# Performance work log

Measured on AMD Instinct MI355X. Metric: run time of the kernel, lower is better.

## Reference

```python
import jax, jax.numpy as jnp
import numpy as np
from jax import lax

B, T, C = 8, 2048, 1024
H, N = 16, 64          # n_head, head_size (C = H*N)
FFN = 3584             # dim_ffn = int(1024*3.5//32*32)
HSD = 8.0              # head_size_divisor
EPS = 1e-5


def setup_inputs() -> dict:
    key = jax.random.key(0)
    ks = jax.random.split(key, 24)
    s = 0.02
    return {
        'x': jax.random.normal(ks[0], (B, T, C), jnp.float32),
        'ln0_w': jnp.ones((C,), jnp.float32), 'ln0_b': jnp.zeros((C,), jnp.float32),
        'ln1_w': jnp.ones((C,), jnp.float32), 'ln1_b': jnp.zeros((C,), jnp.float32),
        'ln2_w': jnp.ones((C,), jnp.float32), 'ln2_b': jnp.zeros((C,), jnp.float32),
        'att_tmk': jax.random.uniform(ks[1], (C,), jnp.float32),
        'att_tmv': jax.random.uniform(ks[2], (C,), jnp.float32),
        'att_tmr': jax.random.uniform(ks[3], (C,), jnp.float32),
        'att_tmg': jax.random.uniform(ks[4], (C,), jnp.float32),
        'att_decay': jax.random.uniform(ks[5], (H, N), jnp.float32, -6.0, -1.0),
        'att_faaaa': jax.random.normal(ks[6], (H, N), jnp.float32) * 0.1,
        'att_Wr': jax.random.normal(ks[7], (C, C), jnp.float32) * s,
        'att_Wk': jax.random.normal(ks[8], (C, C), jnp.float32) * s,
        'att_Wv': jax.random.normal(ks[9], (C, C), jnp.float32) * s,
        'att_Wg': jax.random.normal(ks[10], (C, C), jnp.float32) * s,
        'att_Wo': jax.random.normal(ks[11], (C, C), jnp.float32) * s,
        'att_lnx_w': jnp.ones((C,), jnp.float32), 'att_lnx_b': jnp.zeros((C,), jnp.float32),
        'ffn_tmk': jax.random.uniform(ks[12], (C,), jnp.float32),
        'ffn_tmr': jax.random.uniform(ks[13], (C,), jnp.float32),
        'ffn_Wk': jax.random.normal(ks[14], (FFN, C), jnp.float32) * s,
        'ffn_Wr': jax.random.normal(ks[15], (C, C), jnp.float32) * s,
        'ffn_Wv': jax.random.normal(ks[16], (C, FFN), jnp.float32) * s,
    }


def token_shift(x):
    # nn.ZeroPad2d((0,0,1,-1)): shift right by one along T with zero front pad
    return jnp.pad(x, ((0, 0), (1, 0), (0, 0)))[:, :-1, :]


def layer_norm(x, w, b):
    mu = jnp.mean(x, -1, keepdims=True)
    var = jnp.var(x, -1, keepdims=True)
    return (x - mu) * lax.rsqrt(var + EPS) * w + b


def group_norm(x, w, b):
    # GroupNorm(H groups) over channel dim C = H*N
    xg = x.reshape(*x.shape[:-1], H, N)
    mu = jnp.mean(xg, -1, keepdims=True)
    var = jnp.var(xg, -1, keepdims=True)
    xg = (xg - mu) * lax.rsqrt(var + EPS)
    return xg.reshape(x.shape) * w + b


def wkv5(r, k, v, w, u):
    # r,k,v: [B,T,C]; w,u: [H,N]. Per-head decayed linear attention recurrence.
    ew = jnp.exp(-jnp.exp(w))  # [H,N] decay in (0,1)
    rt = r.reshape(B, T, H, N).transpose(1, 0, 2, 3)  # [T,B,H,N]
    kt = k.reshape(B, T, H, N).transpose(1, 0, 2, 3)
    vt = v.reshape(B, T, H, N).transpose(1, 0, 2, 3)

    def step(S, rkv):
        r_, k_, v_ = rkv                                   # [B,H,N]
        a = k_[..., :, None] * v_[..., None, :]            # [B,H,N,N] outer k v^T
        y = jnp.einsum('bhi,bhij->bhj', r_, S + u[:, :, None] * a)
        S = ew[None, :, :, None] * S + a
        return S, y

    S0 = jnp.zeros((B, H, N, N), r.dtype)
    _, ys = lax.scan(step, S0, (rt, kt, vt))               # ys: [T,B,H,N]
    return ys.transpose(1, 0, 2, 3).reshape(B, T, C)


def reference(x, ln0_w, ln0_b, ln1_w, ln1_b, ln2_w, ln2_b,
              att_tmk, att_tmv, att_tmr, att_tmg, att_decay, att_faaaa,
              att_Wr, att_Wk, att_Wv, att_Wg, att_Wo, att_lnx_w, att_lnx_b,
              ffn_tmk, ffn_tmr, ffn_Wk, ffn_Wr, ffn_Wv):
    x = layer_norm(x, ln0_w, ln0_b)  # layer_id == 0

    # --- time-mix (RWKV_Tmix_x052) ---
    xn = layer_norm(x, ln1_w, ln1_b)
    xx = token_shift(xn)
    xk = xn * att_tmk + xx * (1 - att_tmk)
    xv = xn * att_tmv + xx * (1 - att_tmv)
    xr = xn * att_tmr + xx * (1 - att_tmr)
    xg = xn * att_tmg + xx * (1 - att_tmg)
    r = xr @ att_Wr.T
    k = xk @ att_Wk.T
    v = xv @ att_Wv.T
    g = jax.nn.silu(xg @ att_Wg.T)
    y = wkv5(r, k, v, att_decay, att_faaaa)
    y = group_norm(y / HSD, att_lnx_w, att_lnx_b)
    x = x + (y * g) @ att_Wo.T

    # --- channel-mix (RWKV_CMix_x052) ---
    xn = layer_norm(x, ln2_w, ln2_b)
    xx = token_shift(xn)
    xk = xn * ffn_tmk + xx * (1 - ffn_tmk)
    xr = xn * ffn_tmr + xx * (1 - ffn_tmr)
    kf = jnp.square(jax.nn.relu(xk @ ffn_Wk.T))
    kv = kf @ ffn_Wv.T
    x = x + jax.nn.sigmoid(xr @ ffn_Wr.T) * kv
    return x
```

## Files before the change

### kernel.cpp

```cpp
#include <hip/hip_runtime.h>

#define Bq 8
#define Tq 2048
#define Cq 1024
#define Hq 16
#define Nq 64
#define FFNq 3584
#define EPSq 1e-5f

typedef __bf16 bf8v __attribute__((ext_vector_type(8)));
typedef float f32x4 __attribute__((ext_vector_type(4)));

typedef __attribute__((address_space(1))) const unsigned int GU;
typedef __attribute__((address_space(3))) unsigned int LU;

__device__ __forceinline__ void gload16(const unsigned short* g, unsigned short* l) {
    __builtin_amdgcn_global_load_lds((GU*)g, (LU*)l, 16, 0, 0);
}

__device__ __forceinline__ unsigned short f2bf(float f) {
    unsigned u = __float_as_uint(f);
    u += 0x7fffu + ((u >> 16) & 1u);
    return (unsigned short)(u >> 16);
}
__device__ __forceinline__ float bf2f(unsigned short h) {
    return __uint_as_float(((unsigned)h) << 16);
}

__global__ __launch_bounds__(256)
void diag_kernel(float* __restrict__ out, float val) {
    int i = (blockIdx.x * 256 + threadIdx.x) * 4;
    float4 v = make_float4(val, val, val, val);
    *(float4*)(out + i) = v;
}

__global__ __launch_bounds__(256)
void f2bf_all_kernel(const float* __restrict__ s0, const float* __restrict__ s1,
                     const float* __restrict__ s2, const float* __restrict__ s3,
                     const float* __restrict__ s4, const float* __restrict__ s5,
                     const float* __restrict__ s6, const float* __restrict__ s7,
                     unsigned short* __restrict__ d0, unsigned short* __restrict__ d1,
                     unsigned short* __restrict__ d2, unsigned short* __restrict__ d3,
                     unsigned short* __restrict__ d4, unsigned short* __restrict__ d5,
                     unsigned short* __restrict__ d6, unsigned short* __restrict__ d7) {
    int b = blockIdx.x;
    const float* src; unsigned short* dst;
    if      (b < 1024)  { src = s0; dst = d0; }
    else if (b < 2048)  { src = s1; dst = d1; b -= 1024; }
    else if (b < 3072)  { src = s2; dst = d2; b -= 2048; }
    else if (b < 4096)  { src = s3; dst = d3; b -= 3072; }
    else if (b < 5120)  { src = s4; dst = d4; b -= 4096; }
    else if (b < 8704)  { src = s5; dst = d5; b -= 5120; }
    else if (b < 9728)  { src = s6; dst = d6; b -= 8704; }
    else                { src = s7; dst = d7; b -= 9728; }
    int i = (b * 256 + threadIdx.x) * 4;
    float4 v = *(const float4*)(src + i);
    ushort4 o;
    o.x = f2bf(v.x); o.y = f2bf(v.y); o.z = f2bf(v.z); o.w = f2bf(v.w);
    *(ushort4*)(dst + i) = o;
}

__device__ __forceinline__ void blockred2(float& a, float& b, float* sm) {
#pragma unroll
    for (int m = 1; m < 64; m <<= 1) { a += __shfl_xor(a, m); b += __shfl_xor(b, m); }
    const int w = threadIdx.x >> 6;
    __syncthreads();
    if ((threadIdx.x & 63) == 0) { sm[w] = a; sm[4 + w] = b; }
    __syncthreads();
    a = sm[0] + sm[1] + sm[2] + sm[3];
    b = sm[4] + sm[5] + sm[6] + sm[7];
}

__global__ __launch_bounds__(256)
void ln01_kernel(const float* __restrict__ x,
                 const float* __restrict__ w0, const float* __restrict__ b0,
                 const float* __restrict__ w1, const float* __restrict__ b1,
                 float* __restrict__ x0, unsigned short* __restrict__ xn) {
    __shared__ float sm[8];
    const int tok = blockIdx.x, tid = threadIdx.x, c = tid * 4;
    const size_t base = (size_t)tok * Cq + c;
    float4 v = *(const float4*)(x + base);
    float s = v.x + v.y + v.z + v.w;
    float ss = v.x * v.x + v.y * v.y + v.z * v.z + v.w * v.w;
    blockred2(s, ss, sm);
    float mu = s * (1.f / Cq);
    float rstd = rsqrtf(ss * (1.f / Cq) - mu * mu + EPSq);
    float4 wv = *(const float4*)(w0 + c), bv = *(const float4*)(b0 + c);
    float4 e;
    e.x = (v.x - mu) * rstd * wv.x + bv.x;
    e.y = (v.y - mu) * rstd * wv.y + bv.y;
    e.z = (v.z - mu) * rstd * wv.z + bv.z;
    e.w = (v.w - mu) * rstd * wv.w + bv.w;
    *(float4*)(x0 + base) = e;
    s = e.x + e.y + e.z + e.w;
    ss = e.x * e.x + e.y * e.y + e.z * e.z + e.w * e.w;
    blockred2(s, ss, sm);
    mu = s * (1.f / Cq);
    rstd = rsqrtf(ss * (1.f / Cq) - mu * mu + EPSq);
    wv = *(const float4*)(w1 + c); bv = *(const float4*)(b1 + c);
    ushort4 o;
    o.x = f2bf((e.x - mu) * rstd * wv.x + bv.x);
    o.y = f2bf((e.y - mu) * rstd * wv.y + bv.y);
    o.z = f2bf((e.z - mu) * rstd * wv.z + bv.z);
    o.w = f2bf((e.w - mu) * rstd * wv.w + bv.w);
    *(ushort4*)(xn + base) = o;
}

__global__ __launch_bounds__(256)
void ln_kernel(const float* __restrict__ x, const float* __restrict__ w,
               const float* __restrict__ b, unsigned short* __restrict__ out) {
    __shared__ float sm[8];
    const int tok = blockIdx.x, tid = threadIdx.x, c = tid * 4;
    const size_t base = (size_t)tok * Cq + c;
    float4 v = *(const float4*)(x + base);
    float s = v.x + v.y + v.z + v.w;
    float ss = v.x * v.x + v.y * v.y + v.z * v.z + v.w * v.w;
    blockred2(s, ss, sm);
    float mu = s * (1.f / Cq);
    float rstd = rsqrtf(ss * (1.f / Cq) - mu * mu + EPSq);
    float4 wv = *(const float4*)(w + c), bv = *(const float4*)(b + c);
    ushort4 o;
    o.x = f2bf((v.x - mu) * rstd * wv.x + bv.x);
    o.y = f2bf((v.y - mu) * rstd * wv.y + bv.y);
    o.z = f2bf((v.z - mu) * rstd * wv.z + bv.z);
    o.w = f2bf((v.w - mu) * rstd * wv.w + bv.w);
    *(ushort4*)(out + base) = o;
}

__device__ __forceinline__ ushort4 mixpack(float ax, float ay, float az, float aw,
                                           float px, float py, float pz, float pw,
                                           const float4& m) {
    ushort4 o;
    o.x = f2bf(px + m.x * (ax - px));
    o.y = f2bf(py + m.y * (ay - py));
    o.z = f2bf(pz + m.z * (az - pz));
    o.w = f2bf(pw + m.w * (aw - pw));
    return o;
}

__global__ __launch_bounds__(256)
void mix4_kernel(const unsigned short* __restrict__ xn,
                 const float* __restrict__ tmr, const float* __restrict__ tmk,
                 const float* __restrict__ tmv, const float* __restrict__ tmg,
                 ushort4* __restrict__ outR, ushort4* __restrict__ outK,
                 ushort4* __restrict__ outV, ushort4* __restrict__ outG) {
    const int tok = blockIdx.x, tid = threadIdx.x, c = tid * 4;
    const int t = tok & (Tq - 1);
    const size_t base = (size_t)tok * Cq + c;
    ushort4 a = *(const ushort4*)(xn + base);
    ushort4 p = make_ushort4(0, 0, 0, 0);
    if (t) p = *(const ushort4*)(xn + base - Cq);
    float ax = bf2f(a.x), ay = bf2f(a.y), az = bf2f(a.z), aw = bf2f(a.w);
    float px = bf2f(p.x), py = bf2f(p.y), pz = bf2f(p.z), pw = bf2f(p.w);
    const size_t b4 = (size_t)tok * 256 + tid;
    outR[b4] = mixpack(ax, ay, az, aw, px, py, pz, pw, *(const float4*)(tmr + c));
    outK[b4] = mixpack(ax, ay, az, aw, px, py, pz, pw, *(const float4*)(tmk + c));
    outV[b4] = mixpack(ax, ay, az, aw, px, py, pz, pw, *(const float4*)(tmv + c));
    outG[b4] = mixpack(ax, ay, az, aw, px, py, pz, pw, *(const float4*)(tmg + c));
}

__global__ __launch_bounds__(256)
void mix2_kernel(const unsigned short* __restrict__ xn,
                 const float* __restrict__ tmk, const float* __restrict__ tmr,
                 ushort4* __restrict__ outK, ushort4* __restrict__ outR) {
    const int tok = blockIdx.x, tid = threadIdx.x, c = tid * 4;
    const int t = tok & (Tq - 1);
    const size_t base = (size_t)tok * Cq + c;
    ushort4 a = *(const ushort4*)(xn + base);
    ushort4 p = make_ushort4(0, 0, 0, 0);
    if (t) p = *(const ushort4*)(xn + base - Cq);
    float ax = bf2f(a.x), ay = bf2f(a.y), az = bf2f(a.z), aw = bf2f(a.w);
    float px = bf2f(p.x), py = bf2f(p.y), pz = bf2f(p.z), pw = bf2f(p.w);
    const size_t b4 = (size_t)tok * 256 + tid;
    outK[b4] = mixpack(ax, ay, az, aw, px, py, pz, pw, *(const float4*)(tmk + c));
    outR[b4] = mixpack(ax, ay, az, aw, px, py, pz, pw, *(const float4*)(tmr + c));
}

template<int MODE>
__global__ __launch_bounds__(256, 2)
void gemm_bt(const unsigned short* __restrict__ A, const unsigned short* __restrict__ W,
             int K, int N, float* __restrict__ outF, unsigned short* __restrict__ outB,
             const float* __restrict__ res, const unsigned short* __restrict__ sg) {
    __shared__ unsigned short As[128 * 32];
    __shared__ unsigned short Bs[128 * 32];
    const int tid = threadIdx.x;
    const int nn = N >> 7;
    const int per = nn << 4;
    const int gid = blockIdx.x / per;
    const int rem = blockIdx.x - gid * per;
    const int m0 = ((gid << 4) + (rem & 15)) * 128;
    const int n0 = (rem >> 4) * 128;
    const int wv = tid >> 6, lane = tid & 63;
    const int wm = (wv >> 1) * 64, wn = (wv & 1) * 64;
    const int l15 = lane & 15, q = lane >> 4;

    const int srow = wv * 32 + (lane >> 2);
    const int scol = (lane & 3) * 8;
    const unsigned short* Ag0 = A + (size_t)(m0 + srow) * K + scol;
    const unsigned short* Ag1 = A + (size_t)(m0 + srow + 16) * K + scol;
    const unsigned short* Wg0 = W + (size_t)(n0 + srow) * K + scol;
    const unsigned short* Wg1 = W + (size_t)(n0 + srow + 16) * K + scol;
    unsigned short* As0 = &As[(wv * 32) * 32];
    unsigned short* As1 = &As[(wv * 32 + 16) * 32];
    unsigned short* Bs0 = &Bs[(wv * 32) * 32];
    unsigned short* Bs1 = &Bs[(wv * 32 + 16) * 32];

    f32x4 acc[4][4];
#pragma unroll
    for (int mi = 0; mi < 4; ++mi)
#pragma unroll
        for (int ni = 0; ni < 4; ++ni)
            acc[mi][ni] = {0.f, 0.f, 0.f, 0.f};

    for (int k0 = 0; k0 < K; k0 += 32) {
        gload16(Ag0 + k0, As0);
        gload16(Ag1 + k0, As1);
        gload16(Wg0 + k0, Bs0);
        gload16(Wg1 + k0, Bs1);
        __syncthreads();
        bf8v af[4], bfv[4];
#pragma unroll
        for (int mi = 0; mi < 4; ++mi) af[mi] = *(const bf8v*)&As[(wm + mi * 16 + l15) * 32 + q * 8];
#pragma unroll
        for (int ni = 0; ni < 4; ++ni) bfv[ni] = *(const bf8v*)&Bs[(wn + ni * 16 + l15) * 32 + q * 8];
#pragma unroll
        for (int mi = 0; mi < 4; ++mi)
#pragma unroll
            for (int ni = 0; ni < 4; ++ni)
                acc[mi][ni] = __builtin_amdgcn_mfma_f32_16x16x32_bf16(af[mi], bfv[ni], acc[mi][ni], 0, 0, 0);
        __syncthreads();
    }

#pragma unroll
    for (int mi = 0; mi < 4; ++mi)
#pragma unroll
        for (int ni = 0; ni < 4; ++ni)
#pragma unroll
            for (int j = 0; j < 4; ++j) {
                const int row = m0 + wm + mi * 16 + q * 4 + j;
                const int col = n0 + wn + ni * 16 + l15;
                const size_t idx = (size_t)row * N + col;
                const float a = acc[mi][ni][j];
                if (MODE == 1) {
                    outB[idx] = f2bf(a / (1.f + __expf(-a)));
                } else if (MODE == 2) {
                    outF[idx] = res[idx] + a;
                } else if (MODE == 3) {
                    float t = fmaxf(a, 0.f);
                    outB[idx] = f2bf(t * t);
                } else if (MODE == 4) {
                    outB[idx] = f2bf(1.f / (1.f + __expf(-a)));
                } else if (MODE == 5) {
                    outF[idx] = res[idx] + bf2f(sg[idx]) * a;
                } else {
                    outB[idx] = f2bf(a);
                }
            }
}

__global__ __launch_bounds__(256)
void wkv_kernel(const unsigned short* __restrict__ r, const unsigned short* __restrict__ k,
                const unsigned short* __restrict__ v, const unsigned short* __restrict__ g,
                const float* __restrict__ decay, const float* __restrict__ faaaa,
                const float* __restrict__ lnxw, const float* __restrict__ lnxb,
                unsigned short* __restrict__ ao) {
    __shared__ unsigned short rp[64 * 72], km[64 * 72], kdT[64 * 72];
    __shared__ unsigned short VT[64 * 72], Abf[64 * 72], ScT[64 * 72], Gsh[64 * 72];
    __shared__ float Dt[64];
    const int tid = threadIdx.x;
    const int bh = blockIdx.x, b = bh >> 4, h = bh & 15;
    const int tr = tid >> 2, g4 = tid & 3, i0 = g4 * 16;
    const int wv = tid >> 6, lane = tid & 63, l15 = lane & 15, q = lane >> 4;
    const float LOG2E = 1.44269504088896340736f;

    float l2w[16], uu[16];
#pragma unroll
    for (int ii = 0; ii < 16; ++ii) {
        l2w[ii] = -__expf(decay[h * Nq + i0 + ii]) * LOG2E;
        uu[ii] = faaaa[h * Nq + i0 + ii];
    }
    float ewL[4];
#pragma unroll
    for (int jr = 0; jr < 4; ++jr) {
        float lw = -__expf(decay[h * Nq + 16 * wv + q * 4 + jr]) * LOG2E;
        ewL[jr] = exp2f(64.f * lw);
    }
    const int colbase = h * Nq;
    float lwj[4], lbj[4];
#pragma unroll
    for (int nt = 0; nt < 4; ++nt) {
        lwj[nt] = lnxw[colbase + 16 * nt + l15];
        lbj[nt] = lnxb[colbase + 16 * nt + l15];
    }
    f32x4 S[4];
#pragma unroll
    for (int nt = 0; nt < 4; ++nt) S[nt] = {0.f, 0.f, 0.f, 0.f};
    for (int idx = tid; idx < 64 * 72; idx += 256) ScT[idx] = 0;
    __syncthreads();

    const size_t rowbase = (size_t)b * Tq;

    for (int c = 0; c < 32; ++c) {
        const size_t grow = (rowbase + c * 64 + tr) * Cq + colbase + i0;
        unsigned short rs_[16], ks_[16], vs_[16];
        *(uint4*)&rs_[0] = *(const uint4*)(r + grow);
        *(uint4*)&rs_[8] = *(const uint4*)(r + grow + 8);
        *(uint4*)&ks_[0] = *(const uint4*)(k + grow);
        *(uint4*)&ks_[8] = *(const uint4*)(k + grow + 8);
        *(uint4*)&vs_[0] = *(const uint4*)(v + grow);
        *(uint4*)&vs_[8] = *(const uint4*)(v + grow + 8);
        *(uint4*)&Gsh[tr * 72 + i0] = *(const uint4*)(g + grow);
        *(uint4*)&Gsh[tr * 72 + i0 + 8] = *(const uint4*)(g + grow + 8);
        float pd = 0.f;
        const float ftr = (float)tr;
#pragma unroll
        for (int ii = 0; ii < 16; ++ii) {
            float rf = bf2f(rs_[ii]), kf = bf2f(ks_[ii]);
            rp[tr * 72 + i0 + ii] = f2bf(rf * exp2f(ftr * l2w[ii]));
            km[tr * 72 + i0 + ii] = f2bf(kf * exp2f(-(ftr + 1.f) * l2w[ii]));
            kdT[(i0 + ii) * 72 + tr] = f2bf(kf * exp2f((63.f - ftr) * l2w[ii]));
            VT[(i0 + ii) * 72 + tr] = vs_[ii];
            pd += rf * uu[ii] * kf;
        }
        pd += __shfl_xor(pd, 1);
        pd += __shfl_xor(pd, 2);
        if (g4 == 0) Dt[tr] = pd;
        __syncthreads();

        f32x4 accA[4];
#pragma unroll
        for (int nt = 0; nt < 4; ++nt) accA[nt] = {0.f, 0.f, 0.f, 0.f};
#pragma unroll
        for (int ks = 0; ks < 2; ++ks) {
            bf8v a = *(const bf8v*)&rp[(16 * wv + l15) * 72 + ks * 32 + q * 8];
#pragma unroll
            for (int nt = 0; nt < 4; ++nt) {
                bf8v bb = *(const bf8v*)&km[(16 * nt + l15) * 72 + ks * 32 + q * 8];
                accA[nt] = __builtin_amdgcn_mfma_f32_16x16x32_bf16(a, bb, accA[nt], 0, 0, 0);
            }
        }
#pragma unroll
        for (int nt = 0; nt < 4; ++nt)
#pragma unroll
            for (int jr = 0; jr < 4; ++jr) {
                const int t = 16 * wv + q * 4 + jr, s = 16 * nt + l15;
                const float a = accA[nt][jr];
                const float val = (s < t) ? a : ((s == t) ? Dt[t] : 0.f);
                Abf[t * 72 + s] = f2bf(val);
            }

        f32x4 accY[4];
#pragma unroll
        for (int nt = 0; nt < 4; ++nt) accY[nt] = {0.f, 0.f, 0.f, 0.f};
#pragma unroll
        for (int ks = 0; ks < 2; ++ks) {
            bf8v a = *(const bf8v*)&Abf[(16 * wv + l15) * 72 + ks * 32 + q * 8];
#pragma unroll
            for (int nt = 0; nt < 4; ++nt) {
                bf8v bb = *(const bf8v*)&VT[(16 * nt + l15) * 72 + ks * 32 + q * 8];
                accY[nt] = __builtin_amdgcn_mfma_f32_16x16x32_bf16(a, bb, accY[nt], 0, 0, 0);
            }
        }
#pragma unroll
        for (int ks = 0; ks < 2; ++ks) {
            bf8v a = *(const bf8v*)&rp[(16 * wv + l15) * 72 + ks * 32 + q * 8];
#pragma unroll
            for (int nt = 0; nt < 4; ++nt) {
                bf8v bb = *(const bf8v*)&ScT[(16 * nt + l15) * 72 + ks * 32 + q * 8];
                accY[nt] = __builtin_amdgcn_mfma_f32_16x16x32_bf16(a, bb, accY[nt], 0, 0, 0);
            }
        }

        float sum_[4] = {0.f, 0.f, 0.f, 0.f}, sq_[4] = {0.f, 0.f, 0.f, 0.f};
#pragma unroll
        for (int nt = 0; nt < 4; ++nt)
#pragma unroll
            for (int jr = 0; jr < 4; ++jr) {
                float yv = accY[nt][jr] * 0.125f;
                accY[nt][jr] = yv;
                sum_[jr] += yv;
                sq_[jr] += yv * yv;
            }
#pragma unroll
        for (int m = 1; m < 16; m <<= 1)
#pragma unroll
            for (int jr = 0; jr < 4; ++jr) {
                sum_[jr] += __shfl_xor(sum_[jr], m);
                sq_[jr] += __shfl_xor(sq_[jr], m);
            }
        float mu_[4], rstd_[4];
#pragma unroll
        for (int jr = 0; jr < 4; ++jr) {
            mu_[jr] = sum_[jr] * (1.f / Nq);
            rstd_[jr] = rsqrtf(sq_[jr] * (1.f / Nq) - mu_[jr] * mu_[jr] + EPSq);
        }
#pragma unroll
        for (int nt = 0; nt < 4; ++nt)
#pragma unroll
            for (int jr = 0; jr < 4; ++jr) {
                const int t = 16 * wv + q * 4 + jr;
                const float gate = bf2f(Gsh[t * 72 + 16 * nt + l15]);
                const float val = (accY[nt][jr] - mu_[jr]) * rstd_[jr] * lwj[nt] + lbj[nt];
                ao[(rowbase + c * 64 + t) * Cq + colbase + 16 * nt + l15] = f2bf(val * gate);
            }

        f32x4 accU[4];
#pragma unroll
        for (int nt = 0; nt < 4; ++nt) accU[nt] = {0.f, 0.f, 0.f, 0.f};
#pragma unroll
        for (int ks = 0; ks < 2; ++ks) {
            bf8v a = *(const bf8v*)&kdT[(16 * wv + l15) * 72 + ks * 32 + q * 8];
#pragma unroll
            for (int nt = 0; nt < 4; ++nt) {
                bf8v bb = *(const bf8v*)&VT[(16 * nt + l15) * 72 + ks * 32 + q * 8];
                accU[nt] = __builtin_amdgcn_mfma_f32_16x16x32_bf16(a, bb, accU[nt], 0, 0, 0);
            }
        }
        __syncthreads();
#pragma unroll
        for (int nt = 0; nt < 4; ++nt) {
#pragma unroll
            for (int jr = 0; jr < 4; ++jr)
                S[nt][jr] = ewL[jr] * S[nt][jr] + accU[nt][jr];
            ushort4 sc;
            sc.x = f2bf(S[nt][0]); sc.y = f2bf(S[nt][1]);
            sc.z = f2bf(S[nt][2]); sc.w = f2bf(S[nt][3]);
            *(ushort4*)&ScT[(16 * nt + l15) * 72 + 16 * wv + q * 4] = sc;
        }
        __syncthreads();
    }
}

extern "C" void kernel_launch(void* const* d_in, const int* in_sizes, int n_in,
                              void* d_out, int out_size, void* d_ws, size_t ws_size,
                              hipStream_t stream) {
    const float* x     = (const float*)d_in[0];
    const float* ln0w  = (const float*)d_in[1];
    const float* ln0b  = (const float*)d_in[2];
    const float* ln1w  = (const float*)d_in[3];
    const float* ln1b  = (const float*)d_in[4];
    const float* ln2w  = (const float*)d_in[5];
    const float* ln2b  = (const float*)d_in[6];
    const float* atmk  = (const float*)d_in[7];
    const float* atmv  = (const float*)d_in[8];
    const float* atmr  = (const float*)d_in[9];
    const float* atmg  = (const float*)d_in[10];
    const float* decay = (const float*)d_in[11];
    const float* faaaa = (const float*)d_in[12];
    const float* aWr   = (const float*)d_in[13];
    const float* aWk   = (const float*)d_in[14];
    const float* aWv   = (const float*)d_in[15];
    const float* aWg   = (const float*)d_in[16];
    const float* aWo   = (const float*)d_in[17];
    const float* lnxw  = (const float*)d_in[18];
    const float* lnxb  = (const float*)d_in[19];
    const float* ftmk  = (const float*)d_in[20];
    const float* ftmr  = (const float*)d_in[21];
    const float* fWk   = (const float*)d_in[22];
    const float* fWr   = (const float*)d_in[23];
    const float* fWv   = (const float*)d_in[24];

    const size_t MB = 1024ull * 1024ull;
    const size_t WS_NEEDED = 250 * MB;
    dim3 blk(256);

    if (ws_size < WS_NEEDED) {
        diag_kernel<<<out_size / 1024, blk, 0, stream>>>((float*)d_out,
            1000.f + (float)((double)ws_size / (double)MB));
        return;
    }

    char* ws = (char*)d_ws;
    unsigned short* WR  = (unsigned short*)(ws + 0 * MB);
    unsigned short* WK  = (unsigned short*)(ws + 2 * MB);
    unsigned short* WV  = (unsigned short*)(ws + 4 * MB);
    unsigned short* WG  = (unsigned short*)(ws + 6 * MB);
    unsigned short* WO  = (unsigned short*)(ws + 8 * MB);
    unsigned short* FWK = (unsigned short*)(ws + 10 * MB);
    unsigned short* FWR = (unsigned short*)(ws + 17 * MB);
    unsigned short* FWV = (unsigned short*)(ws + 19 * MB);
    unsigned short* XN  = (unsigned short*)(ws + 26 * MB);
    unsigned short* MXR = (unsigned short*)(ws + 58 * MB);
    unsigned short* MXK = (unsigned short*)(ws + 90 * MB);
    unsigned short* MXV = (unsigned short*)(ws + 122 * MB);
    unsigned short* MXG = (unsigned short*)(ws + 154 * MB);
    unsigned short* Rb  = (unsigned short*)(ws + 186 * MB);
    unsigned short* Kb  = (unsigned short*)(ws + 58 * MB);
    unsigned short* Vb  = (unsigned short*)(ws + 90 * MB);
    unsigned short* Gb  = (unsigned short*)(ws + 122 * MB);
    unsigned short* AO  = (unsigned short*)(ws + 154 * MB);
    unsigned short* XK2 = (unsigned short*)(ws + 58 * MB);
    unsigned short* XR2 = (unsigned short*)(ws + 90 * MB);
    unsigned short* KF  = (unsigned short*)(ws + 122 * MB);
    unsigned short* SRb = (unsigned short*)(ws + 26 * MB);
    float*          X0  = (float*)d_out;

    const int NTOK = Bq * Tq;
    dim3 g8(8 * 128), g28(28 * 128);

    f2bf_all_kernel<<<13312, blk, 0, stream>>>(aWr, aWk, aWv, aWg, aWo, fWk, fWr, fWv,
                                               WR, WK, WV, WG, WO, FWK, FWR, FWV);

    ln01_kernel<<<NTOK, blk, 0, stream>>>(x, ln0w, ln0b, ln1w, ln1b, X0, XN);

    mix4_kernel<<<NTOK, blk, 0, stream>>>(XN, atmr, atmk, atmv, atmg,
                                          (ushort4*)MXR, (ushort4*)MXK,
                                          (ushort4*)MXV, (ushort4*)MXG);
    gemm_bt<6><<<g8, blk, 0, stream>>>(MXR, WR, Cq, Cq, nullptr, Rb, nullptr, nullptr);
    gemm_bt<6><<<g8, blk, 0, stream>>>(MXK, WK, Cq, Cq, nullptr, Kb, nullptr, nullptr);
    gemm_bt<6><<<g8, blk, 0, stream>>>(MXV, WV, Cq, Cq, nullptr, Vb, nullptr, nullptr);
    gemm_bt<1><<<g8, blk, 0, stream>>>(MXG, WG, Cq, Cq, nullptr, Gb, nullptr, nullptr);

    wkv_kernel<<<Bq * Hq, blk, 0, stream>>>(Rb, Kb, Vb, Gb, decay, faaaa, lnxw, lnxb, AO);
    gemm_bt<2><<<g8, blk, 0, stream>>>(AO, WO, Cq, Cq, X0, nullptr, X0, nullptr);

    ln_kernel<<<NTOK, blk, 0, stream>>>(X0, ln2w, ln2b, XN);
    mix2_kernel<<<NTOK, blk, 0, stream>>>(XN, ftmk, ftmr, (ushort4*)XK2, (ushort4*)XR2);
    gemm_bt<3><<<g28, blk, 0, stream>>>(XK2, FWK, Cq, FFNq, nullptr, KF, nullptr, nullptr);
    gemm_bt<4><<<g8, blk, 0, stream>>>(XR2, FWR, Cq, Cq, nullptr, SRb, nullptr, nullptr);
    gemm_bt<5><<<g8, blk, 0, stream>>>(KF, FWV, FFNq, Cq, X0, nullptr, X0, SRb);
}
```

Measured before the change: 981.1 us.

## Replace GEMM with 256x256-tile, 4-stage pipelined, swizzled-LDS kernel

Swaps the 128x128 single-buffered GEMM for a 512-thread kernel using 256x256 output tiles, a 4-slot LDS ring that prefetches 3 K-steps ahead with explicit vmcnt waits, and an XOR swizzle on LDS columns to avoid bank conflicts. It also interleaves A/B loads with MFMA halves, raises wave priority around the MFMAs, and remaps block IDs for L2 locality. The aim is to hide global-load latency and cut LDS traffic per FLOP. In exchange it uses far more registers and LDS per block, giving lower occupancy and fewer blocks (256 for the square GEMMs) relative to the CU count.

```diff
diff --git a/kernel.cpp b/kernel.cpp
--- a/kernel.cpp
+++ b/kernel.cpp
@@ -177,68 +177,114 @@
 }
 
 template<int MODE>
-__global__ __launch_bounds__(256, 2)
-void gemm_bt(const unsigned short* __restrict__ A, const unsigned short* __restrict__ W,
+__global__ __launch_bounds__(512, 2)
+void gemm256(const unsigned short* __restrict__ A, const unsigned short* __restrict__ W,
              int K, int N, float* __restrict__ outF, unsigned short* __restrict__ outB,
              const float* __restrict__ res, const unsigned short* __restrict__ sg) {
-    __shared__ unsigned short As[128 * 32];
-    __shared__ unsigned short Bs[128 * 32];
+    __shared__ unsigned short lds[4][2][8192];
     const int tid = threadIdx.x;
-    const int nn = N >> 7;
-    const int per = nn << 4;
-    const int gid = blockIdx.x / per;
-    const int rem = blockIdx.x - gid * per;
-    const int m0 = ((gid << 4) + (rem & 15)) * 128;
-    const int n0 = (rem >> 4) * 128;
-    const int wv = tid >> 6, lane = tid & 63;
-    const int wm = (wv >> 1) * 64, wn = (wv & 1) * 64;
+    const int wid = tid >> 6, lane = tid & 63;
+    const int wr = wid >> 2, wc = wid & 3;
     const int l15 = lane & 15, q = lane >> 4;
 
-    const int srow = wv * 32 + (lane >> 2);
-    const int scol = (lane & 3) * 8;
-    const unsigned short* Ag0 = A + (size_t)(m0 + srow) * K + scol;
-    const unsigned short* Ag1 = A + (size_t)(m0 + srow + 16) * K + scol;
-    const unsigned short* Wg0 = W + (size_t)(n0 + srow) * K + scol;
-    const unsigned short* Wg1 = W + (size_t)(n0 + srow + 16) * K + scol;
-    unsigned short* As0 = &As[(wv * 32) * 32];
-    unsigned short* As1 = &As[(wv * 32 + 16) * 32];
-    unsigned short* Bs0 = &Bs[(wv * 32) * 32];
-    unsigned short* Bs1 = &Bs[(wv * 32 + 16) * 32];
-
-    f32x4 acc[4][4];
-#pragma unroll
-    for (int mi = 0; mi < 4; ++mi)
+    const int nn = N >> 8;
+    const int q8 = gridDim.x >> 3;
+    const int bid = blockIdx.x;
+    const int swz = (bid & 7) * q8 + (bid >> 3);
+    const int m0 = (swz / nn) * 256;
+    const int n0 = (swz % nn) * 256;
+
+    const int d0 = tid * 16, d1 = 8192 + tid * 16;
+    const int p0 = d0 ^ (((d0 >> 6) & 3) << 4);
+    const int p1 = d1 ^ (((d1 >> 6) & 3) << 4);
+    const int r0 = p0 >> 6, c0 = (p0 >> 1) & 31;
+    const int r1 = p1 >> 6, c1 = (p1 >> 1) & 31;
+    const unsigned short* a0 = A + (size_t)(m0 + r0) * K + c0;
+    const unsigned short* a1 = A + (size_t)(m0 + r1) * K + c1;
+    const unsigned short* w0 = W + (size_t)(n0 + r0) * K + c0;
+    const unsigned short* w1 = W + (size_t)(n0 + r1) * K + c1;
+
+    const int cOff = (q ^ (l15 & 3)) * 8;
+    const int aBase = (wr * 128 + l15) * 32 + cOff;
+    const int bBase = (wc * 64 + l15) * 32 + cOff;
+
+    f32x4 acc[8][4];
+#pragma unroll
+    for (int mi = 0; mi < 8; ++mi)
 #pragma unroll
         for (int ni = 0; ni < 4; ++ni)
             acc[mi][ni] = {0.f, 0.f, 0.f, 0.f};
 
-    for (int k0 = 0; k0 < K; k0 += 32) {
-        gload16(Ag0 + k0, As0);
-        gload16(Ag1 + k0, As1);
-        gload16(Wg0 + k0, Bs0);
-        gload16(Wg1 + k0, Bs1);
-        __syncthreads();
-        bf8v af[4], bfv[4];
-#pragma unroll
-        for (int mi = 0; mi < 4; ++mi) af[mi] = *(const bf8v*)&As[(wm + mi * 16 + l15) * 32 + q * 8];
-#pragma unroll
-        for (int ni = 0; ni < 4; ++ni) bfv[ni] = *(const bf8v*)&Bs[(wn + ni * 16 + l15) * 32 + q * 8];
+    const int NT = K >> 5;
+
+#pragma unroll
+    for (int t = 0; t < 3; ++t) {
+        unsigned short* La = (unsigned short*)&lds[t][0][wid * 512];
+        unsigned short* Lb = (unsigned short*)&lds[t][1][wid * 512];
+        gload16(a0, La); gload16(a1, La + 4096);
+        gload16(w0, Lb); gload16(w1, Lb + 4096);
+        a0 += 32; a1 += 32; w0 += 32; w1 += 32;
+    }
+    asm volatile("s_waitcnt vmcnt(8)" ::: "memory");
+    __builtin_amdgcn_s_barrier();
+
+    for (int t = 0; t < NT; ++t) {
+        const int slot = t & 3;
+        const bool st = (t + 3) < NT;
+        const int ps = (t + 3) & 3;
+        bf8v af[4], bb[4];
+
 #pragma unroll
         for (int mi = 0; mi < 4; ++mi)
+            af[mi] = *(const bf8v*)&lds[slot][0][aBase + mi * 512];
+#pragma unroll
+        for (int ni = 0; ni < 4; ++ni)
+            bb[ni] = *(const bf8v*)&lds[slot][1][bBase + ni * 512];
+        if (st) {
+            unsigned short* La = (unsigned short*)&lds[ps][0][wid * 512];
+            gload16(a0, La); gload16(a1, La + 4096);
+            a0 += 32; a1 += 32;
+        }
+        __builtin_amdgcn_s_barrier();
+        __builtin_amdgcn_s_setprio(1);
+#pragma unroll
+        for (int mi = 0; mi < 4; ++mi)
 #pragma unroll
             for (int ni = 0; ni < 4; ++ni)
-                acc[mi][ni] = __builtin_amdgcn_mfma_f32_16x16x32_bf16(af[mi], bfv[ni], acc[mi][ni], 0, 0, 0);
-        __syncthreads();
-    }
-
-#pragma unroll
-    for (int mi = 0; mi < 4; ++mi)
+                acc[mi][ni] = __builtin_amdgcn_mfma_f32_16x16x32_bf16(af[mi], bb[ni], acc[mi][ni], 0, 0, 0);
+        __builtin_amdgcn_s_setprio(0);
+        __builtin_amdgcn_s_barrier();
+
+#pragma unroll
+        for (int mi = 0; mi < 4; ++mi)
+            af[mi] = *(const bf8v*)&lds[slot][0][aBase + (4 + mi) * 512];
+        if (st) {
+            unsigned short* Lb = (unsigned short*)&lds[ps][1][wid * 512];
+            gload16(w0, Lb); gload16(w1, Lb + 4096);
+            w0 += 32; w1 += 32;
+        }
+        __builtin_amdgcn_s_barrier();
+        __builtin_amdgcn_s_setprio(1);
+#pragma unroll
+        for (int mi = 0; mi < 4; ++mi)
+#pragma unroll
+            for (int ni = 0; ni < 4; ++ni)
+                acc[4 + mi][ni] = __builtin_amdgcn_mfma_f32_16x16x32_bf16(af[mi], bb[ni], acc[4 + mi][ni], 0, 0, 0);
+        __builtin_amdgcn_s_setprio(0);
+        if (t < NT - 3)       { asm volatile("s_waitcnt vmcnt(8)" ::: "memory"); }
+        else if (t == NT - 3) { asm volatile("s_waitcnt vmcnt(4)" ::: "memory"); }
+        else if (t == NT - 2) { asm volatile("s_waitcnt vmcnt(0)" ::: "memory"); }
+        __builtin_amdgcn_s_barrier();
+    }
+
+#pragma unroll
+    for (int mi = 0; mi < 8; ++mi)
 #pragma unroll
         for (int ni = 0; ni < 4; ++ni)
 #pragma unroll
             for (int j = 0; j < 4; ++j) {
-                const int row = m0 + wm + mi * 16 + q * 4 + j;
-                const int col = n0 + wn + ni * 16 + l15;
+                const int row = m0 + wr * 128 + mi * 16 + q * 4 + j;
+                const int col = n0 + wc * 64 + ni * 16 + l15;
                 const size_t idx = (size_t)row * N + col;
                 const float a = acc[mi][ni][j];
                 if (MODE == 1) {
@@ -246,8 +292,8 @@
                 } else if (MODE == 2) {
                     outF[idx] = res[idx] + a;
                 } else if (MODE == 3) {
-                    float t = fmaxf(a, 0.f);
-                    outB[idx] = f2bf(t * t);
+                    float tt = fmaxf(a, 0.f);
+                    outB[idx] = f2bf(tt * tt);
                 } else if (MODE == 4) {
                     outB[idx] = f2bf(1.f / (1.f + __expf(-a)));
                 } else if (MODE == 5) {
@@ -335,8 +381,8 @@
             bf8v a = *(const bf8v*)&rp[(16 * wv + l15) * 72 + ks * 32 + q * 8];
 #pragma unroll
             for (int nt = 0; nt < 4; ++nt) {
-                bf8v bb = *(const bf8v*)&km[(16 * nt + l15) * 72 + ks * 32 + q * 8];
-                accA[nt] = __builtin_amdgcn_mfma_f32_16x16x32_bf16(a, bb, accA[nt], 0, 0, 0);
+                bf8v bbv = *(const bf8v*)&km[(16 * nt + l15) * 72 + ks * 32 + q * 8];
+                accA[nt] = __builtin_amdgcn_mfma_f32_16x16x32_bf16(a, bbv, accA[nt], 0, 0, 0);
             }
         }
 #pragma unroll
@@ -357,8 +403,8 @@
             bf8v a = *(const bf8v*)&Abf[(16 * wv + l15) * 72 + ks * 32 + q * 8];
 #pragma unroll
             for (int nt = 0; nt < 4; ++nt) {
-                bf8v bb = *(const bf8v*)&VT[(16 * nt + l15) * 72 + ks * 32 + q * 8];
-                accY[nt] = __builtin_amdgcn_mfma_f32_16x16x32_bf16(a, bb, accY[nt], 0, 0, 0);
+                bf8v bbv = *(const bf8v*)&VT[(16 * nt + l15) * 72 + ks * 32 + q * 8];
+                accY[nt] = __builtin_amdgcn_mfma_f32_16x16x32_bf16(a, bbv, accY[nt], 0, 0, 0);
             }
         }
 #pragma unroll
@@ -366,8 +412,8 @@
             bf8v a = *(const bf8v*)&rp[(16 * wv + l15) * 72 + ks * 32 + q * 8];
 #pragma unroll
             for (int nt = 0; nt < 4; ++nt) {
-                bf8v bb = *(const bf8v*)&ScT[(16 * nt + l15) * 72 + ks * 32 + q * 8];
-                accY[nt] = __builtin_amdgcn_mfma_f32_16x16x32_bf16(a, bb, accY[nt], 0, 0, 0);
+                bf8v bbv = *(const bf8v*)&ScT[(16 * nt + l15) * 72 + ks * 32 + q * 8];
+                accY[nt] = __builtin_amdgcn_mfma_f32_16x16x32_bf16(a, bbv, accY[nt], 0, 0, 0);
             }
         }
 
@@ -412,8 +458,8 @@
             bf8v a = *(const bf8v*)&kdT[(16 * wv + l15) * 72 + ks * 32 + q * 8];
 #pragma unroll
             for (int nt = 0; nt < 4; ++nt) {
-                bf8v bb = *(const bf8v*)&VT[(16 * nt + l15) * 72 + ks * 32 + q * 8];
-                accU[nt] = __builtin_amdgcn_mfma_f32_16x16x32_bf16(a, bb, accU[nt], 0, 0, 0);
+                bf8v bbv = *(const bf8v*)&VT[(16 * nt + l15) * 72 + ks * 32 + q * 8];
+                accU[nt] = __builtin_amdgcn_mfma_f32_16x16x32_bf16(a, bbv, accU[nt], 0, 0, 0);
             }
         }
         __syncthreads();
@@ -496,7 +542,9 @@
     float*          X0  = (float*)d_out;
 
     const int NTOK = Bq * Tq;
-    dim3 g8(8 * 128), g28(28 * 128);
+    dim3 blk512(512);
+    const int gsq = (NTOK / 256) * (Cq / 256);
+    const int gup = (NTOK / 256) * (FFNq / 256);
 
     f2bf_all_kernel<<<13312, blk, 0, stream>>>(aWr, aWk, aWv, aWg, aWo, fWk, fWr, fWv,
                                                WR, WK, WV, WG, WO, FWK, FWR, FWV);
@@ -506,17 +554,18 @@
     mix4_kernel<<<NTOK, blk, 0, stream>>>(XN, atmr, atmk, atmv, atmg,
                                           (ushort4*)MXR, (ushort4*)MXK,
                                           (ushort4*)MXV, (ushort4*)MXG);
-    gemm_bt<6><<<g8, blk, 0, stream>>>(MXR, WR, Cq, Cq, nullptr, Rb, nullptr, nullptr);
-    gemm_bt<6><<<g8, blk, 0, stream>>>(MXK, WK, Cq, Cq, nullptr, Kb, nullptr, nullptr);
-    gemm_bt<6><<<g8, blk, 0, stream>>>(MXV, WV, Cq, Cq, nullptr, Vb, nullptr, nullptr);
-    gemm_bt<1><<<g8, blk, 0, stream>>>(MXG, WG, Cq, Cq, nullptr, Gb, nullptr, nullptr);
+
+    gemm256<6><<<gsq, blk512, 0, stream>>>(MXR, WR, Cq, Cq, nullptr, Rb, nullptr, nullptr);
+    gemm256<6><<<gsq, blk512, 0, stream>>>(MXK, WK, Cq, Cq, nullptr, Kb, nullptr, nullptr);
+    gemm256<6><<<gsq, blk512, 0, stream>>>(MXV, WV, Cq, Cq, nullptr, Vb, nullptr, nullptr);
+    gemm256<1><<<gsq, blk512, 0, stream>>>(MXG, WG, Cq, Cq, nullptr, Gb, nullptr, nullptr);
 
     wkv_kernel<<<Bq * Hq, blk, 0, stream>>>(Rb, Kb, Vb, Gb, decay, faaaa, lnxw, lnxb, AO);
-    gemm_bt<2><<<g8, blk, 0, stream>>>(AO, WO, Cq, Cq, X0, nullptr, X0, nullptr);
+    gemm256<2><<<gsq, blk512, 0, stream>>>(AO, WO, Cq, Cq, X0, nullptr, X0, nullptr);
 
     ln_kernel<<<NTOK, blk, 0, stream>>>(X0, ln2w, ln2b, XN);
     mix2_kernel<<<NTOK, blk, 0, stream>>>(XN, ftmk, ftmr, (ushort4*)XK2, (ushort4*)XR2);
-    gemm_bt<3><<<g28, blk, 0, stream>>>(XK2, FWK, Cq, FFNq, nullptr, KF, nullptr, nullptr);
-    gemm_bt<4><<<g8, blk, 0, stream>>>(XR2, FWR, Cq, Cq, nullptr, SRb, nullptr, nullptr);
-    gemm_bt<5><<<g8, blk, 0, stream>>>(KF, FWV, FFNq, Cq, X0, nullptr, X0, SRb);
-}
+    gemm256<3><<<gup, blk512, 0, stream>>>(XK2, FWK, Cq, FFNq, nullptr, KF, nullptr, nullptr);
+    gemm256<4><<<gsq, blk512, 0, stream>>>(XR2, FWR, Cq, Cq, nullptr, SRb, nullptr, nullptr);
+    gemm256<5><<<gsq, blk512, 0, stream>>>(KF, FWV, FFNq, Cq, X0, nullptr, X0, SRb);
+}
```

Result: faster. 939.3 us (-4.3%).
